# Optimization experiments

Measured on AMD Instinct MI355X. Metric: run time of the kernel, lower is better.

Reference implementation:

```python
import jax, jax.numpy as jnp
import numpy as np


def setup_inputs() -> dict:
    key = jax.random.key(0)
    k1, k2 = jax.random.split(key)
    B, H, W, N = 32, 1024, 1024, 96
    output = jax.random.uniform(k1, (B, 1, H, W), dtype=jnp.float32)
    bboxes = jax.random.randint(k2, (B, N, 4), 0, W, dtype=jnp.int32)
    return {"output": output, "bboxes": bboxes}


def reference(output, bboxes):
    # output: [B, 1, H, W] density map; bboxes: [B, N, 4] as (x1, y1, x2, y2).
    B, _, H, W = output.shape
    bb = jnp.clip(bboxes.astype(jnp.int32), 0, W)  # torch: bboxes.long().clip(0, W)
    x = output[:, 0]  # [B, H, W]
    # 2D integral image with zero top/left padding: S[b, i, j] = sum of x[b, :i, :j].
    S = jnp.pad(jnp.cumsum(jnp.cumsum(x, axis=1), axis=2), ((0, 0), (1, 0), (1, 0)))  # [B, H+1, W+1]
    x1, y1, x2, y2 = bb[..., 0], bb[..., 1], bb[..., 2], bb[..., 3]  # each [B, N]
    bidx = jnp.arange(B)[:, None]  # [B, 1] broadcast against [B, N]
    g = lambda yy, xx: S[bidx, yy, xx]
    box_sums = g(y2, x2) - g(y1, x2) - g(y2, x1) + g(y1, x1)  # [B, N]
    # Empty torch slices (x2<=x1 or y2<=y1) sum to 0; mask to match.
    valid = (x2 > x1) & (y2 > y1)
    box_sums = jnp.where(valid, box_sums, jnp.zeros_like(box_sums))
    return jnp.sum(jax.nn.relu(1.0 - box_sums))
```

## Files before the change

kernel.cpp:

```cpp
#include <hip/hip_runtime.h>

#define BATCH 32
#define HDIM 1024
#define WDIM 1024
#define NBOX 96
#define ROWS_PER_BLOCK 16
#define THREADS 256

__global__ void zero_ws_kernel(float* __restrict__ ws) {
    int i = blockIdx.x * blockDim.x + threadIdx.x;
    if (i < BATCH * NBOX) ws[i] = 0.0f;
}

__global__ __launch_bounds__(THREADS) void box_accum_kernel(
    const float* __restrict__ img,
    const int* __restrict__ bboxes,
    float* __restrict__ ws_box) {

    __shared__ float Pinc[WDIM];
    __shared__ float wave_tot[THREADS / 64];

    const int t = threadIdx.x;
    const int lane = t & 63;
    const int wave = t >> 6;

    const int blocks_per_batch = HDIM / ROWS_PER_BLOCK;
    const int b = blockIdx.x / blocks_per_batch;
    const int row0 = (blockIdx.x % blocks_per_batch) * ROWS_PER_BLOCK;

    int x1 = 0, y1 = 0, x2 = 0, y2 = 0;
    const bool owns_box = (t < NBOX);
    if (owns_box) {
        const int4 bb = ((const int4*)bboxes)[b * NBOX + t];
        x1 = min(max(bb.x, 0), WDIM);
        y1 = min(max(bb.y, 0), WDIM);
        x2 = min(max(bb.z, 0), WDIM);
        y2 = min(max(bb.w, 0), WDIM);
    }
    const bool x_valid = owns_box && (x2 > x1);
    float acc = 0.0f;

    const float* rowbase = img + ((size_t)b * HDIM + row0) * WDIM;

    for (int r = 0; r < ROWS_PER_BLOCK; ++r) {
        float4 v = ((const float4*)(rowbase + (size_t)r * WDIM))[t];

        float s0 = v.x;
        float s1 = s0 + v.y;
        float s2 = s1 + v.z;
        float s3 = s2 + v.w;

        float wscan = s3;
        #pragma unroll
        for (int off = 1; off < 64; off <<= 1) {
            float u = __shfl_up(wscan, off, 64);
            if (lane >= off) wscan += u;
        }
        float excl_in_wave = wscan - s3;
        if (lane == 63) wave_tot[wave] = wscan;
        __syncthreads();

        float wave_base = 0.0f;
        #pragma unroll
        for (int w = 0; w < THREADS / 64; ++w)
            wave_base += (w < wave) ? wave_tot[w] : 0.0f;

        float base = wave_base + excl_in_wave;

        float4 pv;
        pv.x = base + s0;
        pv.y = base + s1;
        pv.z = base + s2;
        pv.w = base + s3;
        ((float4*)Pinc)[t] = pv;
        __syncthreads();

        const int i = row0 + r;
        if (x_valid && (y1 <= i) && (i < y2)) {
            float right = Pinc[x2 - 1];
            float left  = (x1 > 0) ? Pinc[x1 - 1] : 0.0f;
            acc += right - left;
        }
        __syncthreads();
    }

    if (owns_box && acc != 0.0f) {
        atomicAdd(&ws_box[b * NBOX + t], acc);
    }
}

__global__ void finalize_kernel(const float* __restrict__ ws_box,
                                const int* __restrict__ bboxes,
                                float* __restrict__ out) {
    __shared__ float red[THREADS / 64];
    const int t = threadIdx.x;
    float local = 0.0f;
    for (int idx = t; idx < BATCH * NBOX; idx += THREADS) {
        const int4 bb = ((const int4*)bboxes)[idx];
        int x1 = min(max(bb.x, 0), WDIM);
        int y1 = min(max(bb.y, 0), WDIM);
        int x2 = min(max(bb.z, 0), WDIM);
        int y2 = min(max(bb.w, 0), WDIM);
        bool valid = (x2 > x1) && (y2 > y1);
        float s = valid ? ws_box[idx] : 0.0f;
        local += fmaxf(1.0f - s, 0.0f);
    }
    #pragma unroll
    for (int off = 32; off > 0; off >>= 1)
        local += __shfl_down(local, off, 64);
    if ((t & 63) == 0) red[t >> 6] = local;
    __syncthreads();
    if (t == 0) {
        float r = 0.0f;
        #pragma unroll
        for (int w = 0; w < THREADS / 64; ++w) r += red[w];
        out[0] = r;
    }
}

extern "C" void kernel_launch(void* const* d_in, const int* in_sizes, int n_in,
                              void* d_out, int out_size, void* d_ws, size_t ws_size,
                              hipStream_t stream) {
    const float* img    = (const float*)d_in[0];
    const int*   bboxes = (const int*)d_in[1];
    float* out = (float*)d_out;
    float* ws_box = (float*)d_ws;

    zero_ws_kernel<<<(BATCH * NBOX + THREADS - 1) / THREADS, THREADS, 0, stream>>>(ws_box);

    const int nblocks = BATCH * HDIM / ROWS_PER_BLOCK;
    box_accum_kernel<<<nblocks, THREADS, 0, stream>>>(img, bboxes, ws_box);

    finalize_kernel<<<1, THREADS, 0, stream>>>(ws_box, bboxes, out);
}
```

Before: 198.5 us.

## Give each wave its own full row scan to eliminate block-level barriers

```diff
diff --git a/kernel.cpp b/kernel.cpp
--- a/kernel.cpp
+++ b/kernel.cpp
@@ -4,8 +4,13 @@
 #define HDIM 1024
 #define WDIM 1024
 #define NBOX 96
-#define ROWS_PER_BLOCK 16
 #define THREADS 256
+#define WAVES_PER_BLOCK (THREADS / 64)
+#define ROWS_PER_WAVE 4
+#define LDS_STRIDE 1088
+#define ZERO_SLOT 1087
+
+__device__ __forceinline__ int padidx(int c) { return c + (c >> 4); }
 
 __global__ void zero_ws_kernel(float* __restrict__ ws) {
     int i = blockIdx.x * blockDim.x + threadIdx.x;
@@ -17,76 +22,80 @@
     const int* __restrict__ bboxes,
     float* __restrict__ ws_box) {
 
-    __shared__ float Pinc[WDIM];
-    __shared__ float wave_tot[THREADS / 64];
+    __shared__ float lds[WAVES_PER_BLOCK * LDS_STRIDE];
 
     const int t = threadIdx.x;
     const int lane = t & 63;
     const int wave = t >> 6;
+    float* __restrict__ P = lds + wave * LDS_STRIDE;
 
-    const int blocks_per_batch = HDIM / ROWS_PER_BLOCK;
-    const int b = blockIdx.x / blocks_per_batch;
-    const int row0 = (blockIdx.x % blocks_per_batch) * ROWS_PER_BLOCK;
+    const int gwave = blockIdx.x * WAVES_PER_BLOCK + wave;
+    const int row0 = gwave * ROWS_PER_WAVE;
+    const int b = row0 / HDIM;
+    const int hrow0 = row0 - b * HDIM;
 
-    int x1 = 0, y1 = 0, x2 = 0, y2 = 0;
-    const bool owns_box = (t < NBOX);
-    if (owns_box) {
-        const int4 bb = ((const int4*)bboxes)[b * NBOX + t];
-        x1 = min(max(bb.x, 0), WDIM);
-        y1 = min(max(bb.y, 0), WDIM);
-        x2 = min(max(bb.z, 0), WDIM);
-        y2 = min(max(bb.w, 0), WDIM);
+    if (lane == 0) P[ZERO_SLOT] = 0.0f;
+
+    const int4* __restrict__ bb = (const int4*)bboxes + b * NBOX;
+    int y1a = 0, y2a = 0, ra = 0, la = ZERO_SLOT;
+    int y1b = 0, y2b = 0, rb = 0, lb = ZERO_SLOT;
+    bool va = false, vb = false;
+    {
+        int4 q = bb[lane];
+        int x1 = min(max(q.x, 0), WDIM), x2 = min(max(q.z, 0), WDIM);
+        y1a = min(max(q.y, 0), WDIM);  y2a = min(max(q.w, 0), WDIM);
+        va = (x2 > x1);
+        if (va) { ra = padidx(x2 - 1); la = (x1 > 0) ? padidx(x1 - 1) : ZERO_SLOT; }
     }
-    const bool x_valid = owns_box && (x2 > x1);
-    float acc = 0.0f;
+    if (lane < NBOX - 64) {
+        int4 q = bb[64 + lane];
+        int x1 = min(max(q.x, 0), WDIM), x2 = min(max(q.z, 0), WDIM);
+        y1b = min(max(q.y, 0), WDIM);  y2b = min(max(q.w, 0), WDIM);
+        vb = (x2 > x1);
+        if (vb) { rb = padidx(x2 - 1); lb = (x1 > 0) ? padidx(x1 - 1) : ZERO_SLOT; }
+    }
 
-    const float* rowbase = img + ((size_t)b * HDIM + row0) * WDIM;
+    float acca = 0.0f, accb = 0.0f;
+    const float* rowptr = img + (size_t)row0 * WDIM + lane * 16;
 
-    for (int r = 0; r < ROWS_PER_BLOCK; ++r) {
-        float4 v = ((const float4*)(rowbase + (size_t)r * WDIM))[t];
+    for (int r = 0; r < ROWS_PER_WAVE; ++r) {
+        const float4* lp = (const float4*)(rowptr + (size_t)r * WDIM);
+        float4 v0 = lp[0], v1 = lp[1], v2 = lp[2], v3 = lp[3];
 
-        float s0 = v.x;
-        float s1 = s0 + v.y;
-        float s2 = s1 + v.z;
-        float s3 = s2 + v.w;
+        float p[16];
+        p[0]  = v0.x;        p[1]  = p[0]  + v0.y;
+        p[2]  = p[1] + v0.z; p[3]  = p[2]  + v0.w;
+        p[4]  = p[3] + v1.x; p[5]  = p[4]  + v1.y;
+        p[6]  = p[5] + v1.z; p[7]  = p[6]  + v1.w;
+        p[8]  = p[7] + v2.x; p[9]  = p[8]  + v2.y;
+        p[10] = p[9] + v2.z; p[11] = p[10] + v2.w;
+        p[12] = p[11]+ v3.x; p[13] = p[12] + v3.y;
+        p[14] = p[13]+ v3.z; p[15] = p[14] + v3.w;
 
-        float wscan = s3;
+        float T = p[15];
+        float wscan = T;
         #pragma unroll
         for (int off = 1; off < 64; off <<= 1) {
             float u = __shfl_up(wscan, off, 64);
             if (lane >= off) wscan += u;
         }
-        float excl_in_wave = wscan - s3;
-        if (lane == 63) wave_tot[wave] = wscan;
-        __syncthreads();
+        float E = wscan - T;
 
-        float wave_base = 0.0f;
+        const int base = 17 * lane;
         #pragma unroll
-        for (int w = 0; w < THREADS / 64; ++w)
-            wave_base += (w < wave) ? wave_tot[w] : 0.0f;
+        for (int j = 0; j < 16; ++j) P[base + j] = E + p[j];
 
-        float base = wave_base + excl_in_wave;
+        __builtin_amdgcn_wave_barrier();
 
-        float4 pv;
-        pv.x = base + s0;
-        pv.y = base + s1;
-        pv.z = base + s2;
-        pv.w = base + s3;
-        ((float4*)Pinc)[t] = pv;
-        __syncthreads();
+        const int row = hrow0 + r;
+        if (va && (y1a <= row) && (row < y2a)) acca += P[ra] - P[la];
+        if (vb && (y1b <= row) && (row < y2b)) accb += P[rb] - P[lb];
 
-        const int i = row0 + r;
-        if (x_valid && (y1 <= i) && (i < y2)) {
-            float right = Pinc[x2 - 1];
-            float left  = (x1 > 0) ? Pinc[x1 - 1] : 0.0f;
-            acc += right - left;
-        }
-        __syncthreads();
+        __builtin_amdgcn_wave_barrier();
     }
 
-    if (owns_box && acc != 0.0f) {
-        atomicAdd(&ws_box[b * NBOX + t], acc);
-    }
+    if (va && acca != 0.0f) atomicAdd(&ws_box[b * NBOX + lane], acca);
+    if (vb && accb != 0.0f) atomicAdd(&ws_box[b * NBOX + 64 + lane], accb);
 }
 
 __global__ void finalize_kernel(const float* __restrict__ ws_box,
@@ -96,11 +105,9 @@
     const int t = threadIdx.x;
     float local = 0.0f;
     for (int idx = t; idx < BATCH * NBOX; idx += THREADS) {
-        const int4 bb = ((const int4*)bboxes)[idx];
-        int x1 = min(max(bb.x, 0), WDIM);
-        int y1 = min(max(bb.y, 0), WDIM);
-        int x2 = min(max(bb.z, 0), WDIM);
-        int y2 = min(max(bb.w, 0), WDIM);
+        const int4 q = ((const int4*)bboxes)[idx];
+        int x1 = min(max(q.x, 0), WDIM), y1 = min(max(q.y, 0), WDIM);
+        int x2 = min(max(q.z, 0), WDIM), y2 = min(max(q.w, 0), WDIM);
         bool valid = (x2 > x1) && (y2 > y1);
         float s = valid ? ws_box[idx] : 0.0f;
         local += fmaxf(1.0f - s, 0.0f);
@@ -128,7 +135,7 @@
 
     zero_ws_kernel<<<(BATCH * NBOX + THREADS - 1) / THREADS, THREADS, 0, stream>>>(ws_box);
 
-    const int nblocks = BATCH * HDIM / ROWS_PER_BLOCK;
+    const int nblocks = BATCH * HDIM / (ROWS_PER_WAVE * WAVES_PER_BLOCK);
     box_accum_kernel<<<nblocks, THREADS, 0, stream>>>(img, bboxes, ws_box);
 
     finalize_kernel<<<1, THREADS, 0, stream>>>(ws_box, bboxes, out);
```

Result: no change. 198.7 us (+0.1%).
